# Performance work log

Hardware: AMD Instinct MI355X
Metric: run time of the kernel (lower is better)

The kernel has to match this reference:

```python
import jax, jax.numpy as jnp
import numpy as np


def setup_inputs() -> dict:
    key = jax.random.key(0)
    k1, k2, k3, k4, k5 = jax.random.split(key, 5)
    B, L, D = 8, 4096, 64
    return {
        "Q": jax.random.normal(k1, (B, L, D), dtype=jnp.float32),
        "K": jax.random.normal(k2, (B, L, D), dtype=jnp.float32),
        "V": jax.random.normal(k3, (B, L, D), dtype=jnp.float32),
        "sent_embed_slice": jax.random.normal(k4, (B, D), dtype=jnp.float32),
        "proj": jax.random.normal(k5, (D, D), dtype=jnp.float32),  # fixed phi projection (M, d)
        "qkv_size": 64,
        "masked": 1,
    }


def _phi(X, proj, M):
    # X: (B, L, d). Original applies phi per timestep slice x = X[:, t, :] of shape (B, d)
    # phi(x) = (1/sqrt(M)) * exp(-0.5 * ||x||_F) * exp(proj @ x), Frobenius norm over the (B, d) slice.
    logits = jnp.einsum("bld,md->blm", X, proj)            # (B, L, M)
    scale = jnp.exp(-0.5 * jnp.sqrt(jnp.sum(X * X, axis=(0, 2))))  # per-timestep scalar, (L,)
    return jnp.exp(logits) * scale[None, :, None] / jnp.sqrt(jnp.asarray(M, jnp.float32))


def reference(Q, K, V, sent_embed_slice, proj, qkv_size, masked):
    M = qkv_size
    phi_q = _phi(Q, proj, M)  # (B, L, M)
    phi_k = _phi(K, proj, M)  # (B, L, M)
    if masked:
        # causal running sums: KV_t = sum_{j<=t} phi_k_j outer V_j ; N_t = sum_{j<=t} phi_k_j
        KV = jnp.cumsum(phi_k[:, :, :, None] * V[:, :, None, :], axis=1)  # (B, L, M, D)
        Nc = jnp.cumsum(phi_k, axis=1)                                    # (B, L, M)
        num = jnp.einsum("blm,blmd->bld", phi_q, KV)
        r = jnp.einsum("blm,blm->bl", phi_q, Nc)
        return num / (r + jnp.sign(r) * 1e-6)[:, :, None]
    else:
        KV = jnp.einsum("blm,bld->bmd", phi_k, V)     # (B, M, D)
        Ns = jnp.sum(phi_k, axis=1)                    # (B, M); broadcast over D like torch norm_sum
        num = jnp.einsum("blm,bmd->bld", phi_q, KV)
        r = jnp.einsum("blm,bm->bl", phi_q, Ns)
        return num / r[:, :, None]
```

## Files before the change

### kernel.cpp

```cpp
#include <hip/hip_runtime.h>
#include <math.h>

#define BB 8
#define LL 4096
#define DD 64
#define SS 64
#define NCHUNK 64
#define STATE 4160

typedef __attribute__((ext_vector_type(8))) short s16x8;
typedef __attribute__((ext_vector_type(8))) unsigned short u16x8;
typedef __attribute__((ext_vector_type(4))) float f32x4;

#define MFMA(a, b, c) __builtin_amdgcn_mfma_f32_16x16x32_bf16((a), (b), (c), 0, 0, 0)

static __device__ __forceinline__ unsigned short f2bf(float x) {
  unsigned int u = __builtin_bit_cast(unsigned int, x);
  u += 0x7FFFu + ((u >> 16) & 1u);
  return (unsigned short)(u >> 16);
}
static __device__ __forceinline__ float bf2f(unsigned short h) {
  unsigned int u = ((unsigned int)h) << 16;
  return __builtin_bit_cast(float, u);
}

static __device__ __forceinline__ s16x8 ld_frag(const unsigned short* base, int row0, int ks) {
  const int lane = threadIdx.x & 63;
  const int r = row0 + (lane & 15);
  const int idx = r * 64 + ((ks * 32 + ((lane & 48) >> 1)) ^ ((r & 7) << 3));
  return *(const s16x8*)(base + idx);
}

static __device__ __forceinline__ void stage_hl(unsigned short* __restrict__ Sh,
                                                unsigned short* __restrict__ Sl,
                                                const float* __restrict__ src, int tid) {
#pragma unroll
  for (int it = 0; it < 2; ++it) {
    const int g = tid + it * 256;
    const int row = g >> 3;
    const int c0 = (g & 7) * 8;
    const float4 x0 = *(const float4*)(src + row * 64 + c0);
    const float4 x1 = *(const float4*)(src + row * 64 + c0 + 4);
    const float xs[8] = {x0.x, x0.y, x0.z, x0.w, x1.x, x1.y, x1.z, x1.w};
    u16x8 h, l;
#pragma unroll
    for (int k = 0; k < 8; ++k) {
      const unsigned short hh = f2bf(xs[k]);
      h[k] = hh;
      l[k] = f2bf(xs[k] - bf2f(hh));
    }
    const int idx = row * 64 + (c0 ^ ((row & 7) << 3));
    *(u16x8*)(Sh + idx) = h;
    *(u16x8*)(Sl + idx) = l;
  }
}

static __device__ __forceinline__ void stage_img(unsigned short* __restrict__ S,
                                                 const unsigned short* __restrict__ src, int tid) {
#pragma unroll
  for (int it = 0; it < 2; ++it) {
    const int g = tid + it * 256;
    const int row = g >> 3;
    const int c0 = (g & 7) * 8;
    *(u16x8*)(S + row * 64 + (c0 ^ ((row & 7) << 3))) = *(const u16x8*)(src + row * 64 + c0);
  }
}

static __device__ __forceinline__ void vtrans_half_g(unsigned short* __restrict__ Gh,
                                                     unsigned short* __restrict__ Hl,
                                                     const float* __restrict__ Vt, int tid, int half) {
  const int d = tid & 63;
  const int tb = (tid >> 6) * 8;
  float v[8];
#pragma unroll
  for (int k = 0; k < 8; ++k) v[k] = Vt[(half * 32 + tb + k) * 64 + d];
  u16x8 hh, ll;
#pragma unroll
  for (int k = 0; k < 8; ++k) {
    const unsigned short h = f2bf(v[k]);
    hh[k] = h;
    ll[k] = f2bf(v[k] - bf2f(h));
  }
  const int idx = d * 64 + ((half * 32 + tb) ^ ((d & 7) << 3));
  *(u16x8*)(Gh + idx) = hh;
  *(u16x8*)(Hl + idx) = ll;
}

static __device__ __forceinline__ void logits3(const unsigned short* Ah_, const unsigned short* Al_,
                                               const unsigned short* Bh_, const unsigned short* Bl_,
                                               int w, f32x4 acc[4]) {
  s16x8 ah[2], al[2];
#pragma unroll
  for (int ks = 0; ks < 2; ++ks) {
    ah[ks] = ld_frag(Ah_, w * 16, ks);
    al[ks] = ld_frag(Al_, w * 16, ks);
  }
#pragma unroll
  for (int ct = 0; ct < 4; ++ct) {
#pragma unroll
    for (int ks = 0; ks < 2; ++ks) {
      const s16x8 bh = ld_frag(Bh_, ct * 16, ks);
      const s16x8 bl = ld_frag(Bl_, ct * 16, ks);
      acc[ct] = MFMA(ah[ks], bh, acc[ct]);
      acc[ct] = MFMA(ah[ks], bl, acc[ct]);
      acc[ct] = MFMA(al[ks], bh, acc[ct]);
    }
  }
}

static __device__ __forceinline__ void phi_store_row(unsigned short* dst, const f32x4* acc,
                                                     const float* sc, int w) {
  const int lane = threadIdx.x & 63;
#pragma unroll
  for (int ri = 0; ri < 4; ++ri) {
    const int t = w * 16 + ((lane & 48) >> 2) + ri;
#pragma unroll
    for (int ct = 0; ct < 4; ++ct) {
      const int m = ct * 16 + (lane & 15);
      dst[t * 64 + (m ^ ((t & 7) << 3))] = f2bf(__expf(acc[ct][ri]) * sc[ri]);
    }
  }
}

static __device__ __forceinline__ void phi_store_col(unsigned short* dst, const f32x4* acc,
                                                     const float* sc, int w) {
  const int lane = threadIdx.x & 63;
#pragma unroll
  for (int ri = 0; ri < 4; ++ri) {
    const int t = w * 16 + ((lane & 48) >> 2) + ri;
#pragma unroll
    for (int ct = 0; ct < 4; ++ct) {
      const int m = ct * 16 + (lane & 15);
      dst[m * 64 + (t ^ ((m & 7) << 3))] = f2bf(__expf(acc[ct][ri]) * sc[ri]);
    }
  }
}

__global__ __launch_bounds__(256) void k_scales(const float* __restrict__ Q,
                                                const float* __restrict__ K,
                                                float* __restrict__ ws) {
  const int t = blockIdx.x * 4 + (threadIdx.x >> 6);
  const int lane = threadIdx.x & 63;
  const int b = lane >> 3;
  const int d0 = (lane & 7) * 8;
  const size_t base = (size_t)b * (LL * DD) + (size_t)t * DD + d0;
  const float4 q0 = *(const float4*)(Q + base);
  const float4 q1 = *(const float4*)(Q + base + 4);
  const float4 k0 = *(const float4*)(K + base);
  const float4 k1 = *(const float4*)(K + base + 4);
  float sq = q0.x * q0.x + q0.y * q0.y + q0.z * q0.z + q0.w * q0.w +
             q1.x * q1.x + q1.y * q1.y + q1.z * q1.z + q1.w * q1.w;
  float sk = k0.x * k0.x + k0.y * k0.y + k0.z * k0.z + k0.w * k0.w +
             k1.x * k1.x + k1.y * k1.y + k1.z * k1.z + k1.w * k1.w;
#pragma unroll
  for (int off = 32; off; off >>= 1) {
    sq += __shfl_xor(sq, off);
    sk += __shfl_xor(sk, off);
  }
  if (lane == 0) {
    ws[t]      = expf(-0.5f * sqrtf(sq));
    ws[LL + t] = expf(-0.5f * sqrtf(sk));
  }
}

__global__ __launch_bounds__(256) void k_chunk_sums(const float* __restrict__ Kg,
                                                    const float* __restrict__ Vg,
                                                    const float* __restrict__ proj,
                                                    const float* __restrict__ ws,
                                                    float* __restrict__ states,
                                                    unsigned short* __restrict__ phiKg) {
  __shared__ unsigned short A_[4096], B_[4096];
  __shared__ unsigned short C_[4096], D_[4096];
  __shared__ unsigned short E_[4096];
  __shared__ unsigned short G_[4096], H_[4096];
  __shared__ unsigned short R_[4096];
  const int tid = threadIdx.x;
  const int lane = tid & 63;
  const int w = tid >> 6;
  const int bc = blockIdx.x;
  const int b = bc >> 6;
  const int c = bc & (NCHUNK - 1);
  const int t0 = c * SS;
  const size_t tileBase = ((size_t)b * LL + t0) * DD;
  float* stc = states + ((size_t)b * NCHUNK + c) * (size_t)STATE;
  unsigned short* pkT = phiKg + (size_t)bc * 4096;

  stage_hl(A_, B_, proj, tid);
  stage_hl(C_, D_, Kg + tileBase, tid);
  float sck[4];
#pragma unroll
  for (int ri = 0; ri < 4; ++ri) {
    const int trow = w * 16 + ((lane & 48) >> 2) + ri;
    sck[ri] = ws[LL + t0 + trow] * 0.125f;
  }
  __syncthreads();

  {
    f32x4 acc[4] = {};
    logits3(C_, D_, A_, B_, w, acc);
    phi_store_col(E_, acc, sck, w);
    phi_store_row(R_, acc, sck, w);
  }
  vtrans_half_g(G_, H_, Vg + tileBase, tid, 0);
  vtrans_half_g(G_, H_, Vg + tileBase, tid, 1);
  __syncthreads();

  {
    const int r0 = tid >> 3;
    const int c0 = (tid & 7) * 8;
#pragma unroll
    for (int it = 0; it < 2; ++it) {
      const int r = r0 + it * 32;
      const int sidx = r * 64 + (c0 ^ ((r & 7) << 3));
      *(u16x8*)(pkT + r * 64 + c0) = *(const u16x8*)(R_ + sidx);
    }
  }
  {
    const int m = tid >> 2, q = tid & 3;
    float s = 0.f;
#pragma unroll
    for (int p = 0; p < 2; ++p) {
      const int tt = q * 16 + p * 8;
      const u16x8 vv = *(const u16x8*)(E_ + m * 64 + (tt ^ ((m & 7) << 3)));
#pragma unroll
      for (int i = 0; i < 8; ++i) s += bf2f(vv[i]);
    }
    s += __shfl_xor(s, 1);
    s += __shfl_xor(s, 2);
    if (q == 0) stc[4096 + m] = s;
  }
  {
    s16x8 avh[2], avl[2];
#pragma unroll
    for (int ks = 0; ks < 2; ++ks) {
      avh[ks] = ld_frag(G_, w * 16, ks);
      avl[ks] = ld_frag(H_, w * 16, ks);
    }
    f32x4 acc[4] = {};
#pragma unroll
    for (int ct = 0; ct < 4; ++ct)
#pragma unroll
      for (int ks = 0; ks < 2; ++ks) {
        const s16x8 bp = ld_frag(E_, ct * 16, ks);
        acc[ct] = MFMA(avh[ks], bp, acc[ct]);
        acc[ct] = MFMA(avl[ks], bp, acc[ct]);
      }
#pragma unroll
    for (int ri = 0; ri < 4; ++ri) {
      const int d = w * 16 + ((lane & 48) >> 2) + ri;
#pragma unroll
      for (int ct = 0; ct < 4; ++ct) {
        stc[d * 64 + ct * 16 + (lane & 15)] = acc[ct][ri];
      }
    }
  }
}

__global__ __launch_bounds__(256) void k_prefix1(const float* __restrict__ states,
                                                 float* __restrict__ tmp) {
  const int e = blockIdx.x * 256 + threadIdx.x;
  if (e >= BB * 8 * STATE) return;
  const int b = e / (8 * STATE);
  const int r = e % (8 * STATE);
  const int g = r / STATE;
  const int el = r % STATE;
  const float* p = states + ((size_t)b * NCHUNK + g * 8) * STATE + el;
  float s = 0.f;
#pragma unroll
  for (int i = 0; i < 8; ++i) s += p[(size_t)i * STATE];
  tmp[((size_t)b * 8 + g) * STATE + el] = s;
}

__global__ __launch_bounds__(256) void k_prefix2(float* __restrict__ states,
                                                 const float* __restrict__ tmp) {
  const int e = blockIdx.x * 256 + threadIdx.x;
  if (e >= BB * 8 * STATE) return;
  const int b = e / (8 * STATE);
  const int r = e % (8 * STATE);
  const int g = r / STATE;
  const int el = r % STATE;
  float run = 0.f;
  for (int g2 = 0; g2 < g; ++g2) run += tmp[((size_t)b * 8 + g2) * STATE + el];
  float* p = states + ((size_t)b * NCHUNK + g * 8) * STATE + el;
#pragma unroll
  for (int i = 0; i < 8; ++i) {
    const float v = p[(size_t)i * STATE];
    p[(size_t)i * STATE] = run;
    run += v;
  }
}

__global__ __launch_bounds__(256) void k_out(const float* __restrict__ Qg,
                                             const float* __restrict__ Vg,
                                             const float* __restrict__ proj,
                                             const unsigned short* __restrict__ phiKg,
                                             const float* __restrict__ ws,
                                             const float* __restrict__ states,
                                             float* __restrict__ out) {
  __shared__ unsigned short A_[4096], B_[4096];
  __shared__ unsigned short C_[4096];
  __shared__ unsigned short D_[4096];
  __shared__ unsigned short PK[4096];
  __shared__ unsigned short KV0[4096], KV1[4096];
  const int tid = threadIdx.x;
  const int lane = tid & 63;
  const int w = tid >> 6;
  const int bc = blockIdx.x;
  const int b = bc >> 6;
  const int c = bc & (NCHUNK - 1);
  const int t0 = c * SS;
  const size_t tileBase = ((size_t)b * LL + t0) * DD;
  const float* st = states + ((size_t)b * NCHUNK + c) * (size_t)STATE;
  const unsigned short* pkT = phiKg + (size_t)bc * 4096;

  stage_hl(A_, B_, proj, tid);
  stage_hl(C_, D_, Qg + tileBase, tid);
  stage_img(PK, pkT, tid);
  stage_hl(KV0, KV1, st, tid);
  float scq[4];
#pragma unroll
  for (int ri = 0; ri < 4; ++ri) {
    const int trow = w * 16 + ((lane & 48) >> 2) + ri;
    scq[ri] = ws[t0 + trow] * 0.125f;
  }
  __syncthreads();

  s16x8 aq[2];
  {
    f32x4 acc[4] = {};
    logits3(C_, D_, A_, B_, w, acc);
    phi_store_row(C_, acc, scq, w);
#pragma unroll
    for (int ks = 0; ks < 2; ++ks) aq[ks] = ld_frag(C_, w * 16, ks);
  }
  __syncthreads();

  vtrans_half_g(A_, B_, Vg + tileBase, tid, 0);
  vtrans_half_g(A_, B_, Vg + tileBase, tid, 1);

  float rsI[4];
  {
    f32x4 accA[4] = {};
#pragma unroll
    for (int ct = 0; ct < 4; ++ct)
#pragma unroll
      for (int ks = 0; ks < 2; ++ks)
        accA[ct] = MFMA(aq[ks], ld_frag(PK, ct * 16, ks), accA[ct]);
#pragma unroll
    for (int ri = 0; ri < 4; ++ri) {
      const int t = w * 16 + ((lane & 48) >> 2) + ri;
      float part = 0.f;
#pragma unroll
      for (int ct = 0; ct < 4; ++ct) {
        const int j = ct * 16 + (lane & 15);
        const float a = (j <= t) ? accA[ct][ri] : 0.f;
        const unsigned short ah = f2bf(a);
        part += bf2f(ah);
        D_[t * 64 + (j ^ ((t & 7) << 3))] = ah;
      }
#pragma unroll
      for (int off = 1; off < 16; off <<= 1) part += __shfl_xor(part, off);
      rsI[ri] = part;
    }
  }
  __syncthreads();

  {
    s16x8 aA[2];
#pragma unroll
    for (int ks = 0; ks < 2; ++ks) aA[ks] = ld_frag(D_, w * 16, ks);
    f32x4 acc[4] = {};
#pragma unroll
    for (int ct = 0; ct < 4; ++ct) {
#pragma unroll
      for (int ks = 0; ks < 2; ++ks) {
        acc[ct] = MFMA(aA[ks], ld_frag(A_, ct * 16, ks), acc[ct]);
        acc[ct] = MFMA(aA[ks], ld_frag(B_, ct * 16, ks), acc[ct]);
        acc[ct] = MFMA(aq[ks], ld_frag(KV0, ct * 16, ks), acc[ct]);
        acc[ct] = MFMA(aq[ks], ld_frag(KV1, ct * 16, ks), acc[ct]);
      }
    }
    float rsp = 0.f;
    const float* Np = st + 4096;
#pragma unroll
    for (int ks = 0; ks < 2; ++ks) {
      const int m0 = ks * 32 + ((lane & 48) >> 1);
      const float4 n0 = *(const float4*)(Np + m0);
      const float4 n1 = *(const float4*)(Np + m0 + 4);
      const float nn[8] = {n0.x, n0.y, n0.z, n0.w, n1.x, n1.y, n1.z, n1.w};
#pragma unroll
      for (int i = 0; i < 8; ++i) rsp += bf2f((unsigned short)aq[ks][i]) * nn[i];
    }
    rsp += __shfl_xor(rsp, 16);
    rsp += __shfl_xor(rsp, 32);
#pragma unroll
    for (int ri = 0; ri < 4; ++ri) {
      const float r = rsI[ri] + __shfl(rsp, ((lane & 48) >> 2) + ri);
      const float inv = 1.f / (r + copysignf(1e-6f, r));
      const int t = w * 16 + ((lane & 48) >> 2) + ri;
#pragma unroll
      for (int ct = 0; ct < 4; ++ct) {
        out[tileBase + t * 64 + ct * 16 + (lane & 15)] = acc[ct][ri] * inv;
      }
    }
  }
}

extern "C" void kernel_launch(void* const* d_in, const int* in_sizes, int n_in,
                              void* d_out, int out_size, void* d_ws, size_t ws_size,
                              hipStream_t stream) {
  (void)in_sizes; (void)n_in; (void)out_size; (void)ws_size;
  const float* Q    = (const float*)d_in[0];
  const float* K    = (const float*)d_in[1];
  const float* V    = (const float*)d_in[2];
  const float* proj = (const float*)d_in[4];
  float* out = (float*)d_out;
  float* ws  = (float*)d_ws;
  float* states = ws + 2 * LL;
  const size_t statesFloats = (size_t)BB * NCHUNK * STATE;
  float* tmp = states + statesFloats;
  const size_t tmpFloats = (size_t)BB * 8 * STATE;
  unsigned short* phiKg = (unsigned short*)(tmp + tmpFloats);

  hipLaunchKernelGGL(k_scales, dim3(LL / 4), dim3(256), 0, stream, Q, K, ws);
  hipLaunchKernelGGL(k_chunk_sums, dim3(BB * NCHUNK), dim3(256), 0, stream,
                     K, V, proj, ws, states, phiKg);
  hipLaunchKernelGGL(k_prefix1, dim3((BB * 8 * STATE + 255) / 256), dim3(256), 0, stream, states, tmp);
  hipLaunchKernelGGL(k_prefix2, dim3((BB * 8 * STATE + 255) / 256), dim3(256), 0, stream, states, tmp);
  hipLaunchKernelGGL(k_out, dim3(BB * NCHUNK), dim3(256), 0, stream,
                     Q, V, proj, phiKg, ws, states, out);
}
```

Baseline: 34.11 us.

## Fuse two-pass chunk prefix into single serial scan and overlap Q scales

Result: slower. 34.85 us (+2.2%).

```diff
diff --git a/kernel.cpp b/kernel.cpp
--- a/kernel.cpp
+++ b/kernel.cpp
@@ -136,31 +136,20 @@
   }
 }
 
-__global__ __launch_bounds__(256) void k_scales(const float* __restrict__ Q,
-                                                const float* __restrict__ K,
-                                                float* __restrict__ ws) {
+__global__ __launch_bounds__(256) void k_scalesK(const float* __restrict__ K,
+                                                 float* __restrict__ ws) {
   const int t = blockIdx.x * 4 + (threadIdx.x >> 6);
   const int lane = threadIdx.x & 63;
   const int b = lane >> 3;
   const int d0 = (lane & 7) * 8;
   const size_t base = (size_t)b * (LL * DD) + (size_t)t * DD + d0;
-  const float4 q0 = *(const float4*)(Q + base);
-  const float4 q1 = *(const float4*)(Q + base + 4);
   const float4 k0 = *(const float4*)(K + base);
   const float4 k1 = *(const float4*)(K + base + 4);
-  float sq = q0.x * q0.x + q0.y * q0.y + q0.z * q0.z + q0.w * q0.w +
-             q1.x * q1.x + q1.y * q1.y + q1.z * q1.z + q1.w * q1.w;
   float sk = k0.x * k0.x + k0.y * k0.y + k0.z * k0.z + k0.w * k0.w +
              k1.x * k1.x + k1.y * k1.y + k1.z * k1.z + k1.w * k1.w;
 #pragma unroll
-  for (int off = 32; off; off >>= 1) {
-    sq += __shfl_xor(sq, off);
-    sk += __shfl_xor(sk, off);
-  }
-  if (lane == 0) {
-    ws[t]      = expf(-0.5f * sqrtf(sq));
-    ws[LL + t] = expf(-0.5f * sqrtf(sk));
-  }
+  for (int off = 32; off; off >>= 1) sk += __shfl_xor(sk, off);
+  if (lane == 0) ws[LL + t] = expf(-0.5f * sqrtf(sk));
 }
 
 __global__ __launch_bounds__(256) void k_chunk_sums(const float* __restrict__ Kg,
@@ -256,36 +245,36 @@
   }
 }
 
-__global__ __launch_bounds__(256) void k_prefix1(const float* __restrict__ states,
-                                                 float* __restrict__ tmp) {
-  const int e = blockIdx.x * 256 + threadIdx.x;
-  if (e >= BB * 8 * STATE) return;
-  const int b = e / (8 * STATE);
-  const int r = e % (8 * STATE);
-  const int g = r / STATE;
-  const int el = r % STATE;
-  const float* p = states + ((size_t)b * NCHUNK + g * 8) * STATE + el;
-  float s = 0.f;
-#pragma unroll
-  for (int i = 0; i < 8; ++i) s += p[(size_t)i * STATE];
-  tmp[((size_t)b * 8 + g) * STATE + el] = s;
-}
-
-__global__ __launch_bounds__(256) void k_prefix2(float* __restrict__ states,
-                                                 const float* __restrict__ tmp) {
-  const int e = blockIdx.x * 256 + threadIdx.x;
-  if (e >= BB * 8 * STATE) return;
-  const int b = e / (8 * STATE);
-  const int r = e % (8 * STATE);
-  const int g = r / STATE;
-  const int el = r % STATE;
+#define NQBLK (LL / 4)
+__global__ __launch_bounds__(256) void k_prefix_fused(const float* __restrict__ Q,
+                                                      float* __restrict__ states,
+                                                      float* __restrict__ ws) {
+  const int tid = threadIdx.x;
+  if (blockIdx.x < NQBLK) {
+    const int t = blockIdx.x * 4 + (tid >> 6);
+    const int lane = tid & 63;
+    const int b = lane >> 3;
+    const int d0 = (lane & 7) * 8;
+    const size_t base = (size_t)b * (LL * DD) + (size_t)t * DD + d0;
+    const float4 q0 = *(const float4*)(Q + base);
+    const float4 q1 = *(const float4*)(Q + base + 4);
+    float sq = q0.x * q0.x + q0.y * q0.y + q0.z * q0.z + q0.w * q0.w +
+               q1.x * q1.x + q1.y * q1.y + q1.z * q1.z + q1.w * q1.w;
+#pragma unroll
+    for (int off = 32; off; off >>= 1) sq += __shfl_xor(sq, off);
+    if (lane == 0) ws[t] = expf(-0.5f * sqrtf(sq));
+    return;
+  }
+  const int e = (blockIdx.x - NQBLK) * 256 + tid;
+  if (e >= BB * STATE) return;
+  const int b = e / STATE;
+  const int el = e % STATE;
+  float* p = states + (size_t)b * NCHUNK * STATE + el;
   float run = 0.f;
-  for (int g2 = 0; g2 < g; ++g2) run += tmp[((size_t)b * 8 + g2) * STATE + el];
-  float* p = states + ((size_t)b * NCHUNK + g * 8) * STATE + el;
-#pragma unroll
-  for (int i = 0; i < 8; ++i) {
-    const float v = p[(size_t)i * STATE];
-    p[(size_t)i * STATE] = run;
+#pragma unroll 4
+  for (int c = 0; c < NCHUNK; ++c) {
+    const float v = p[(size_t)c * STATE];
+    p[(size_t)c * STATE] = run;
     run += v;
   }
 }
@@ -422,11 +411,12 @@
   const size_t tmpFloats = (size_t)BB * 8 * STATE;
   unsigned short* phiKg = (unsigned short*)(tmp + tmpFloats);
 
-  hipLaunchKernelGGL(k_scales, dim3(LL / 4), dim3(256), 0, stream, Q, K, ws);
+  const int prefixBlocks = (BB * STATE + 255) / 256;
+  hipLaunchKernelGGL(k_scalesK, dim3(LL / 4), dim3(256), 0, stream, K, ws);
   hipLaunchKernelGGL(k_chunk_sums, dim3(BB * NCHUNK), dim3(256), 0, stream,
                      K, V, proj, ws, states, phiKg);
-  hipLaunchKernelGGL(k_prefix1, dim3((BB * 8 * STATE + 255) / 256), dim3(256), 0, stream, states, tmp);
-  hipLaunchKernelGGL(k_prefix2, dim3((BB * 8 * STATE + 255) / 256), dim3(256), 0, stream, states, tmp);
+  hipLaunchKernelGGL(k_prefix_fused, dim3(NQBLK + prefixBlocks), dim3(256), 0, stream,
+                     Q, states, ws);
   hipLaunchKernelGGL(k_out, dim3(BB * NCHUNK), dim3(256), 0, stream,
                      Q, V, proj, phiKg, ws, states, out);
 }
```
